# Optimization experiments

Hardware: AMD Instinct MI355X
Metric: run time of the kernel (lower is better)

The kernel has to match this reference:

```python
import jax, jax.numpy as jnp
import numpy as np

H = 512          # hidden_dim
D = 128          # input_dim
L = 8            # output_dim == NUMLABELS
T = 64           # encoder time steps per frame-feature sequence
W = 240          # WINDOWWIDTH (encoder batch dim, one element per frame)
CTX = W // 4     # 60 attention positions
NSTEPS = W // 8


def _lstm(x, Wih, Whh, bih, bhh):
    """PyTorch-convention LSTM (gate order i,f,g,o). x: (T,B,Din) -> (outputs (T,B,H), final h (B,H))."""
    B = x.shape[1]
    Hh = Whh.shape[1]
    xp = jnp.einsum('tbd,gd->tbg', x, Wih) + bih + bhh  # fold both biases
    def step(carry, g):
        h, c = carry
        g = g + h @ Whh.T
        i, f, gg, o = jnp.split(g, 4, axis=-1)
        c = jax.nn.sigmoid(f) * c + jax.nn.sigmoid(i) * jnp.tanh(gg)
        h = jax.nn.sigmoid(o) * jnp.tanh(c)
        return (h, c), h
    z = jnp.zeros((B, Hh), x.dtype)
    (hT, _), hs = jax.lax.scan(step, (z, z), xp)
    return hs, hT


def _forward(data, enc_Wih, enc_Whh, enc_bih, enc_bhh,
             p1f_Wih, p1f_Whh, p1f_bih, p1f_bhh, p1b_Wih, p1b_Whh, p1b_bih, p1b_bhh,
             p2f_Wih, p2f_Whh, p2f_bih, p2f_bhh, p2b_Wih, p2b_Whh, p2b_bih, p2b_bhh,
             attn_W, attn_b, comb_W, comb_b,
             gru_Wih, gru_Whh, gru_bih, gru_bhh, out_W, out_b):
    # --- encoder: per-frame LSTM over T steps, keep final hidden per frame ---
    _, h_enc = _lstm(data, enc_Wih, enc_Whh, enc_bih, enc_bhh)          # (W, H)
    # --- pyramidal bi-LSTM 1: pairs of frames ---
    x1 = h_enc.reshape(W // 2, 1, 2 * H)
    f1, _ = _lstm(x1, p1f_Wih, p1f_Whh, p1f_bih, p1f_bhh)
    b1, _ = _lstm(x1[::-1], p1b_Wih, p1b_Whh, p1b_bih, p1b_bhh)
    # --- pyramidal bi-LSTM 2 ---
    x2 = jnp.concatenate([f1, b1[::-1]], axis=-1).reshape(W // 4, 1, 4 * H)
    f2, h2T = _lstm(x2, p2f_Wih, p2f_Whh, p2f_bih, p2f_bhh)
    b2, _ = _lstm(x2[::-1], p2b_Wih, p2b_Whh, p2b_bih, p2b_bhh)
    ctx = jnp.concatenate([f2, b2[::-1]], axis=-1).reshape(CTX, 2 * H)  # (60, 2H)
    h = h2T[0]                                   # forward-direction final hidden, (H,)
    inp0 = jnp.zeros((L,), data.dtype).at[L - 1].set(1.0)  # one_hot(NOLABEL)

    def dec_step(carry, _):
        inp, h = carry
        aw = jax.nn.softmax(attn_W @ jnp.concatenate([inp, h]) + attn_b)    # (60,)
        applied = aw @ ctx                                                   # (2H,)
        o = jax.nn.relu(comb_W @ jnp.concatenate([inp, applied]) + comb_b)  # (H,)
        # PyTorch GRU cell (gate order r,z,n)
        gi = gru_Wih @ o + gru_bih
        gh = gru_Whh @ h + gru_bhh
        ir, iz, inn = jnp.split(gi, 3)
        hr, hz, hn = jnp.split(gh, 3)
        r = jax.nn.sigmoid(ir + hr)
        z = jax.nn.sigmoid(iz + hz)
        n = jnp.tanh(inn + r * hn)
        h_new = (1.0 - z) * n + z * h
        logp = jax.nn.log_softmax(out_W @ h_new + out_b)                     # (L,)
        return (logp, h_new), logp  # prediction feeds back as next input (y=None path)

    _, outputs = jax.lax.scan(dec_step, (inp0, h), None, length=NSTEPS)
    return outputs  # (30, L)


def setup_inputs() -> dict:
    key = jax.random.key(0)
    ks = iter(jax.random.split(key, 64))
    def mk(*shape):
        return (jax.random.normal(next(ks), shape) * 0.05).astype(jnp.float32)
    d = {"data": jax.random.normal(next(ks), (T, W, D), dtype=jnp.float32)}
    d.update(enc_Wih=mk(4 * H, D), enc_Whh=mk(4 * H, H), enc_bih=mk(4 * H), enc_bhh=mk(4 * H))
    for p, din in (("p1f", 2 * H), ("p1b", 2 * H), ("p2f", 4 * H), ("p2b", 4 * H)):
        d[p + "_Wih"] = mk(4 * H, din)
        d[p + "_Whh"] = mk(4 * H, H)
        d[p + "_bih"] = mk(4 * H)
        d[p + "_bhh"] = mk(4 * H)
    d.update(attn_W=mk(CTX, H + L), attn_b=mk(CTX), comb_W=mk(H, 2 * H + L), comb_b=mk(H),
             gru_Wih=mk(3 * H, H), gru_Whh=mk(3 * H, H), gru_bih=mk(3 * H), gru_bhh=mk(3 * H),
             out_W=mk(L, H), out_b=mk(L))
    return d


def reference(data, enc_Wih, enc_Whh, enc_bih, enc_bhh,
              p1f_Wih, p1f_Whh, p1f_bih, p1f_bhh, p1b_Wih, p1b_Whh, p1b_bih, p1b_bhh,
              p2f_Wih, p2f_Whh, p2f_bih, p2f_bhh, p2b_Wih, p2b_Whh, p2b_bih, p2b_bhh,
              attn_W, attn_b, comb_W, comb_b,
              gru_Wih, gru_Whh, gru_bih, gru_bhh, out_W, out_b):
    return _forward(data, enc_Wih, enc_Whh, enc_bih, enc_bhh,
                    p1f_Wih, p1f_Whh, p1f_bih, p1f_bhh, p1b_Wih, p1b_Whh, p1b_bih, p1b_bhh,
                    p2f_Wih, p2f_Whh, p2f_bih, p2f_bhh, p2b_Wih, p2b_Whh, p2b_bih, p2b_bhh,
                    attn_W, attn_b, comb_W, comb_b,
                    gru_Wih, gru_Whh, gru_bih, gru_bhh, out_W, out_b)
```

## Files before the change

kernel.cpp:

```cpp
#include <hip/hip_runtime.h>
#include <math.h>


typedef __attribute__((ext_vector_type(8))) short short8;
typedef __attribute__((ext_vector_type(4))) float floatx4;
typedef unsigned long long ull;

__device__ __forceinline__ float sigf(float x) { return 1.f / (1.f + __expf(-x)); }
__device__ __forceinline__ float tanh_f(float x) {
    float e = __expf(2.f * x);
    return 1.f - 2.f / (e + 1.f);
}
__device__ __forceinline__ unsigned short f2b(float x) {
    unsigned u = __float_as_uint(x);
    unsigned r = (u + 0x7FFFu + ((u >> 16) & 1u)) >> 16;
    return (unsigned short)r;
}

__device__ __forceinline__ float gld(const float* p) {
    return __hip_atomic_load(p, __ATOMIC_RELAXED, __HIP_MEMORY_SCOPE_AGENT);
}
__device__ __forceinline__ void gst(float* p, float v) {
    __hip_atomic_store(p, v, __ATOMIC_RELAXED, __HIP_MEMORY_SCOPE_AGENT);
}
__device__ __forceinline__ ull gldll(const ull* p) {
    return __hip_atomic_load(p, __ATOMIC_RELAXED, __HIP_MEMORY_SCOPE_AGENT);
}
__device__ __forceinline__ void gstll(ull* p, ull v) {
    __hip_atomic_store(p, v, __ATOMIC_RELAXED, __HIP_MEMORY_SCOPE_AGENT);
}
__device__ __forceinline__ ull packfe(float d, int ep) {
    return ((ull)(unsigned)ep << 32) | (ull)__float_as_uint(d);
}
__device__ __forceinline__ float lowf(ull v) { return __uint_as_float((unsigned)v); }

__global__ void init_k(float* __restrict__ ws) {
    for (int i = blockIdx.x * blockDim.x + threadIdx.x; i < 501760; i += gridDim.x * blockDim.x)
        ws[i] = 0.f;
}

__global__ void __launch_bounds__(256, 1) enc_all(
    const float* __restrict__ data,
    const float* __restrict__ Wih, const float* __restrict__ Whh,
    const float* __restrict__ bih, const float* __restrict__ bhh,
    ull* __restrict__ fastF,
    ull* __restrict__ hbufF,
    float* __restrict__ henc)
{
    __shared__ short act2[20 * 64 * 8];
    __shared__ float gw[4][640];
    __shared__ float cs[512];
    __shared__ short hw[4][16][8];
    __shared__ float biasL[4][4][8];

    const int tid = threadIdx.x;
    const int xcd = blockIdx.x & 7, kk = blockIdx.x >> 3;
    const int fg = xcd * 2 + (kk >> 4), ds = kk & 15;
    if (fg >= 15) return;

    const int w = tid >> 6, lane = tid & 63;
    const int n = lane & 15, q = lane >> 4;

    short8 bfrag[2][20];
#pragma unroll
    for (int nt = 0; nt < 2; ++nt) {
        int rr = nt * 16 + n;
        int g = rr >> 3, dp = rr & 7;
        int grow = g * 512 + ds * 32 + w * 8 + dp;
#pragma unroll
        for (int kt = 0; kt < 20; ++kt) {
            int k0 = kt * 32 + q * 8;
            const float* src = (k0 < 512) ? (Whh + (size_t)grow * 512 + k0)
                                          : (Wih + (size_t)grow * 128 + (k0 - 512));
            float4 lo = *(const float4*)src;
            float4 hi = *(const float4*)(src + 4);
            short8 bf;
            bf[0] = (short)f2b(lo.x); bf[1] = (short)f2b(lo.y);
            bf[2] = (short)f2b(lo.z); bf[3] = (short)f2b(lo.w);
            bf[4] = (short)f2b(hi.x); bf[5] = (short)f2b(hi.y);
            bf[6] = (short)f2b(hi.z); bf[7] = (short)f2b(hi.w);
            bfrag[nt][kt] = bf;
        }
    }
    if (tid < 128) {
        int w2 = tid >> 5, rr = tid & 31;
        int g = rr >> 3, dp = rr & 7;
        int grow = g * 512 + ds * 32 + w2 * 8 + dp;
        biasL[w2][g][dp] = bih[grow] + bhh[grow];
    }
    for (int i = tid; i < 512; i += 256) cs[i] = 0.f;
    __syncthreads();

    unsigned* a2u = (unsigned*)act2;

    for (int t = 0; t < 64; ++t) {
        const int kt2 = tid >> 6, l2 = tid & 63, f2v = l2 & 15, q2 = l2 >> 4;
        const float* xs = data + ((size_t)t * 240 + fg * 16 + f2v) * 128 + kt2 * 32 + q2 * 8;
        float4 lo = *(const float4*)xs;
        float4 hi = *(const float4*)(xs + 4);

        {
            const size_t goff = (size_t)((t & 1) * 15 + fg) * 4096;
            const ull* fsrc = fastF + goff;
            const ull* ssrc = hbufF + goff;
            ull v[16];
            for (;;) {
                bool ok = true;
#pragma unroll
                for (int k2 = 0; k2 < 16; ++k2) {
                    v[k2] = *(volatile const ull*)(fsrc + tid + 256 * k2);
                    ok &= ((int)(v[k2] >> 32) == t);
                }
                if (ok) break;
                ok = true;
#pragma unroll
                for (int k2 = 0; k2 < 16; ++k2) {
                    v[k2] = gldll(ssrc + tid + 256 * k2);
                    ok &= ((int)(v[k2] >> 32) == t);
                }
                if (ok) break;
                __builtin_amdgcn_s_sleep(1);
            }
#pragma unroll
            for (int k2 = 0; k2 < 16; ++k2)
                a2u[tid + 256 * k2] = (unsigned)v[k2];
        }
        {
            short8 xp;
            xp[0] = (short)f2b(lo.x); xp[1] = (short)f2b(lo.y);
            xp[2] = (short)f2b(lo.z); xp[3] = (short)f2b(lo.w);
            xp[4] = (short)f2b(hi.x); xp[5] = (short)f2b(hi.y);
            xp[6] = (short)f2b(hi.z); xp[7] = (short)f2b(hi.w);
            *(short8*)&act2[((16 + kt2) * 64 + l2) * 8] = xp;
        }
        __syncthreads();

        floatx4 acc0 = {0.f, 0.f, 0.f, 0.f};
        floatx4 acc1 = {0.f, 0.f, 0.f, 0.f};
#pragma unroll
        for (int kt = 0; kt < 20; ++kt) {
            short8 a = *(short8*)&act2[(kt * 64 + lane) * 8];
            acc0 = __builtin_amdgcn_mfma_f32_16x16x32_bf16(a, bfrag[0][kt], acc0, 0, 0, 0);
            acc1 = __builtin_amdgcn_mfma_f32_16x16x32_bf16(a, bfrag[1][kt], acc1, 0, 0, 0);
        }
        *(floatx4*)&gw[w][(0 * 16 + n) * 20 + 4 * q] = acc0;
        *(floatx4*)&gw[w][(1 * 16 + n) * 20 + 4 * q] = acc1;

        int nb = (t + 1) & 1;
#pragma unroll
        for (int it = 0; it < 2; ++it) {
            int f = lane & 15, dp = q + 4 * it;
            float gi = gw[w][(0 * 8 + dp) * 20 + f] + biasL[w][0][dp];
            float gf = gw[w][(1 * 8 + dp) * 20 + f] + biasL[w][1][dp];
            float gg = gw[w][(2 * 8 + dp) * 20 + f] + biasL[w][2][dp];
            float go = gw[w][(3 * 8 + dp) * 20 + f] + biasL[w][3][dp];
            int ci = f * 32 + w * 8 + dp;
            float cc = cs[ci];
            float cn = sigf(gf) * cc + sigf(gi) * tanh_f(gg);
            float hn = sigf(go) * tanh_f(cn);
            cs[ci] = cn;
            hw[w][f][dp] = (short)f2b(hn);
            if (t == 63)
                gst(&henc[(size_t)(fg * 16 + f) * 512 + ds * 32 + w * 8 + dp], hn);
        }
        if (lane < 16) {
            const unsigned* hwu = (const unsigned*)&hw[w][lane][0];
            size_t off = (size_t)(nb * 15 + fg) * 4096 + (ds * 64 + w * 16 + lane) * 4;
            ull* fdst = fastF + off;
            ull* sdst = hbufF + off;
            const ull ep = ((ull)(unsigned)(t + 1)) << 32;
#pragma unroll
            for (int r = 0; r < 4; ++r) {
                ull wv = ep | (ull)hwu[r];
                *(volatile ull*)(fdst + r) = wv;
                gstll(sdst + r, wv);
            }
        }
        __syncthreads();
    }
}

__global__ void __launch_bounds__(256) gemm_xp2(
    const float* __restrict__ A, int M, int K, int halfgrid,
    const float* __restrict__ WvF, const float* __restrict__ baF,
    const float* __restrict__ bbF, float* __restrict__ CF,
    const float* __restrict__ WvB, const float* __restrict__ baB,
    const float* __restrict__ bbB, float* __restrict__ CB)
{
    __shared__ float At[16][66];
    __shared__ float Wt[128][66];
    const int tid = threadIdx.x;
    int bgl = blockIdx.x;
    const int rev = (bgl >= halfgrid) ? 1 : 0;
    if (rev) bgl -= halfgrid;
    const float* Wv = rev ? WvB : WvF;
    const float* ba = rev ? baB : baF;
    const float* bb = rev ? bbB : bbF;
    float* C        = rev ? CB : CF;

    const int nt = bgl & 15, mt = bgl >> 4;
    const int rp = tid >> 2, fq = tid & 3;
    const int lr0 = 2 * rp, lr1 = lr0 + 1;
    const int n0 = nt * 128 + lr0, n1 = n0 + 1;

    float acc0[4], acc1[4];
    {
        float b0 = ba[n0] + bb[n0], b1 = ba[n1] + bb[n1];
#pragma unroll
        for (int j = 0; j < 4; ++j) { acc0[j] = b0; acc1[j] = b1; }
    }

    for (int kt = 0; kt < K; kt += 64) {
        {
            int f = tid >> 4, c4 = tid & 15;
            int m = mt * 16 + f;
            float4 v = make_float4(0.f, 0.f, 0.f, 0.f);
            if (m < M) {
                int ar = rev ? (M - 1 - m) : m;
                v = ((const float4*)(A + (size_t)ar * K + kt))[c4];
            }
            At[f][c4 * 4 + 0] = v.x; At[f][c4 * 4 + 1] = v.y;
            At[f][c4 * 4 + 2] = v.z; At[f][c4 * 4 + 3] = v.w;
        }
        for (int i = tid; i < 2048; i += 256) {
            int lr = i >> 4, c4 = i & 15;
            float4 v = ((const float4*)(Wv + (size_t)(nt * 128 + lr) * K + kt))[c4];
            Wt[lr][c4 * 4 + 0] = v.x; Wt[lr][c4 * 4 + 1] = v.y;
            Wt[lr][c4 * 4 + 2] = v.z; Wt[lr][c4 * 4 + 3] = v.w;
        }
        __syncthreads();
        const float2* w0p = (const float2*)(&Wt[lr0][0]);
        const float2* w1p = (const float2*)(&Wt[lr1][0]);
#pragma unroll 8
        for (int kh = 0; kh < 32; ++kh) {
            float2 w0 = w0p[kh], w1 = w1p[kh];
#pragma unroll
            for (int j = 0; j < 4; ++j) {
                float2 av = ((const float2*)(&At[4 * fq + j][0]))[kh];
                acc0[j] += w0.x * av.x + w0.y * av.y;
                acc1[j] += w1.x * av.x + w1.y * av.y;
            }
        }
        __syncthreads();
    }
#pragma unroll
    for (int j = 0; j < 4; ++j) {
        int m = mt * 16 + 4 * fq + j;
        if (m < M) {
            C[(size_t)m * 2048 + n0] = acc0[j];
            C[(size_t)m * 2048 + n1] = acc1[j];
        }
    }
}

__global__ void __launch_bounds__(256, 1) pyr_rec(
    const float* __restrict__ xpF, const float* __restrict__ xpB,
    const float* __restrict__ WhhF, const float* __restrict__ WhhB,
    ull* __restrict__ hp,
    float* __restrict__ outF, float* __restrict__ outB,
    int steps)
{
    const int tid = threadIdx.x;
    const int dir = blockIdx.x >> 6, blk = blockIdx.x & 63;
    const float* xp  = dir ? xpB : xpF;
    const float* Whh = dir ? WhhB : WhhF;
    float* outp = dir ? outB : outF;
    ull* hpd = hp + (size_t)dir * 1024;

    __shared__ __align__(16) float hcur[512];
    __shared__ float red[32][9];
    __shared__ float gv[32];

    const int lr = tid & 31, seg = tid >> 5;
    const int grow = (lr >> 3) * 512 + blk * 8 + (lr & 7);
    float4 wl4[16];
#pragma unroll
    for (int j = 0; j < 16; ++j)
        wl4[j] = *(const float4*)&Whh[(size_t)grow * 512 + 4 * seg + 32 * j];

    const int growx = (tid >> 3) * 512 + blk * 8 + (tid & 7);
    float creg = 0.f;
    __syncthreads();

    for (int t = 0; t < steps; ++t) {
        float xg = 0.f;
        if (tid < 32) xg = xp[(size_t)t * 2048 + growx];
        {
            const ull* base = hpd + (size_t)(t & 1) * 512;
            ull v0 = gldll(base + tid), v1 = gldll(base + tid + 256);
            while (((int)(v0 >> 32) != t) | ((int)(v1 >> 32) != t)) {
                __builtin_amdgcn_s_sleep(1);
                v0 = gldll(base + tid);
                v1 = gldll(base + tid + 256);
            }
            hcur[tid]       = lowf(v0);
            hcur[tid + 256] = lowf(v1);
        }
        __syncthreads();

        float a = 0.f;
#pragma unroll
        for (int j = 0; j < 16; ++j) {
            float4 w = wl4[j];
            float4 h4 = *(const float4*)&hcur[4 * seg + 32 * j];
            a += w.x*h4.x + w.y*h4.y + w.z*h4.z + w.w*h4.w;
        }
        red[lr][seg] = a;
        __syncthreads();

        if (tid < 32) {
            float g = xg;
#pragma unroll
            for (int s2 = 0; s2 < 8; ++s2) g += red[tid][s2];
            gv[tid] = g;
        }
        __syncthreads();
        if (tid < 8) {
            float i_ = sigf(gv[tid]), f_ = sigf(gv[8 + tid]);
            float g_ = tanh_f(gv[16 + tid]), o_ = sigf(gv[24 + tid]);
            creg = f_ * creg + i_ * g_;
            float hn = o_ * tanh_f(creg);
            int d = blk * 8 + tid;
            gstll(&hpd[((t + 1) & 1) * 512 + d], packfe(hn, t + 1));
            int row = dir ? (steps - 1 - t) : t;
            outp[(size_t)row * 512 + d] = hn;
        }
        __syncthreads();
    }
}

__global__ void x2_assemble(const float* __restrict__ f1, const float* __restrict__ b1o,
                            float* __restrict__ x2)
{
    int j = blockIdx.x;
    for (int k = threadIdx.x; k < 2048; k += 256) {
        int q = k >> 9, r = k & 511;
        const float* src = (q & 1) ? b1o : f1;
        int row = 2 * j + (q >> 1);
        x2[(size_t)j * 2048 + k] = src[(size_t)row * 512 + r];
    }
}

__global__ void ctx_k(const float* __restrict__ f2, const float* __restrict__ b2o,
                      float* __restrict__ ctx, ull* __restrict__ hdec_p)
{
    int j = blockIdx.x;
    for (int k = threadIdx.x; k < 1024; k += 256)
        ctx[(size_t)j * 1024 + k] = (k < 512) ? f2[(size_t)j * 512 + k]
                                              : b2o[(size_t)j * 512 + k - 512];
    if (j == 0) {
        for (int i = threadIdx.x; i < 512; i += 256)
            hdec_p[i] = packfe(f2[59 * 512 + i], 0);
    }
}

__global__ void __launch_bounds__(256) precomp_M(
    const float* __restrict__ comb_W,
    const float* __restrict__ ctx,
    float* __restrict__ MgT)
{
    __shared__ float cw[8 * 1024];
    const int tid = threadIdx.x, d0 = blockIdx.x * 8;
    for (int i = tid; i < 2048; i += 256) {
        int r = i >> 8, c4 = i & 255;
        float4 v = *(const float4*)&comb_W[(size_t)(d0 + r) * 1032 + 8 + 4 * c4];
        *(float4*)&cw[r * 1024 + 4 * c4] = v;
    }
    __syncthreads();
    for (int o = tid; o < 480; o += 256) {
        int dl = o / 60, j = o % 60;
        const float4* cp = (const float4*)&cw[dl * 1024];
        const float4* xp = (const float4*)(ctx + (size_t)j * 1024);
        float a = 0.f;
#pragma unroll 4
        for (int k = 0; k < 256; ++k) {
            float4 w = cp[k], x = xp[k];
            a += w.x * x.x + w.y * x.y + w.z * x.z + w.w * x.w;
        }
        MgT[(size_t)j * 512 + (d0 + dl)] = a;
    }
}

__global__ void __launch_bounds__(512, 1) dec_k(
    const float* __restrict__ attn_W, const float* __restrict__ attn_b,
    const float* __restrict__ comb_W, const float* __restrict__ comb_b,
    const float* __restrict__ gWih, const float* __restrict__ gWhh,
    const float* __restrict__ gbih, const float* __restrict__ gbhh,
    const float* __restrict__ outW, const float* __restrict__ outb,
    const float* __restrict__ MgT,
    ull* __restrict__ hdec_p,
    float* __restrict__ dout)
{
    const int tid = threadIdx.x, bid = blockIdx.x;
    const int lane = tid & 63, wv = tid >> 6;
    const int dbase = bid * 8;

    __shared__ float M2T[68][512];
    __shared__ __align__(16) float hL[520];
    __shared__ __align__(16) float xl[512];
    __shared__ __align__(16) float awx[68];
    __shared__ float zd[8], zh[64];
    __shared__ float ghl[24], gil[24];
    __shared__ float biasg[24], biasi[24];
    __shared__ float cbL[512];
    __shared__ float attnbL[64], outbL[8];

    const int rg = tid >> 4, sg = tid & 15;
    const int rz = tid >> 3, szz = tid & 7;

    float4 wo2[2];
    float4 wg8[8], wi8[8];
    float4 wzh[16];
    float4 wip[2];
    {
        const float* wp = outW + (size_t)wv * 512 + 4 * lane;
        wo2[0] = *(const float4*)wp;
        wo2[1] = *(const float4*)(wp + 256);
    }
    {
        int rr = (rg < 24) ? rg : 23;
        size_t grow = (size_t)((rr >> 3) * 512 + dbase + (rr & 7)) * 512 + 4 * sg;
#pragma unroll
        for (int i = 0; i < 8; ++i) {
            wg8[i] = *(const float4*)&gWhh[grow + 64 * i];
            wi8[i] = *(const float4*)&gWih[grow + 64 * i];
        }
    }
    {
        int rr = (rz < 60) ? rz : 59;
        size_t base = (size_t)rr * 520 + 8 + 4 * szz;
#pragma unroll
        for (int i = 0; i < 16; ++i)
            wzh[i] = *(const float4*)&attn_W[base + 32 * i];
    }
    {
        int rr = (tid < 60) ? tid : 59;
        wip[0] = *(const float4*)&attn_W[(size_t)rr * 520 + 0];
        wip[1] = *(const float4*)&attn_W[(size_t)rr * 520 + 4];
    }
    if (tid < 24) {
        int g2 = (tid >> 3) * 512 + dbase + (tid & 7);
        biasg[tid] = gbhh[g2];
        biasi[tid] = gbih[g2];
    }
    cbL[tid] = comb_b[tid];
    if (tid < 64) attnbL[tid] = (tid < 60) ? attn_b[tid] : 0.f;
    if (tid < 8) outbL[tid] = outb[tid];
    for (int i = tid; i < 7680; i += 512) {
        int j = i >> 7, c4 = i & 127;
        *(float4*)&M2T[j][4 * c4] = *(const float4*)&MgT[(size_t)j * 512 + 4 * c4];
    }
    for (int i = tid; i < 4096; i += 512) {
        int r = i >> 3, c = i & 7;
        M2T[60 + c][r] = comb_W[(size_t)r * 1032 + c];
    }
    __syncthreads();

    for (int s = 0; s < 30; ++s) {
        {
            const ull* hs = hdec_p + (size_t)(s & 1) * 512;
            ull v0 = gldll(hs + tid);
            while ((int)(v0 >> 32) != s) {
                __builtin_amdgcn_s_sleep(1);
                v0 = gldll(hs + tid);
            }
            hL[tid] = lowf(v0);
        }
        __syncthreads();

        {
            float a = 0.f;
            float4 h0 = *(const float4*)&hL[4 * lane];
            float4 h1 = *(const float4*)&hL[4 * lane + 256];
            a += wo2[0].x*h0.x + wo2[0].y*h0.y + wo2[0].z*h0.z + wo2[0].w*h0.w;
            a += wo2[1].x*h1.x + wo2[1].y*h1.y + wo2[1].z*h1.z + wo2[1].w*h1.w;
#pragma unroll
            for (int off = 32; off; off >>= 1) a += __shfl_xor(a, off);
            if (lane == 0) zd[wv] = a;
        }
        {
            float a = 0.f;
#pragma unroll
            for (int i = 0; i < 8; ++i) {
                float4 w = wg8[i];
                float4 h4 = *(const float4*)&hL[4 * sg + 64 * i];
                a += w.x*h4.x + w.y*h4.y + w.z*h4.z + w.w*h4.w;
            }
            a += __shfl_xor(a, 1); a += __shfl_xor(a, 2);
            a += __shfl_xor(a, 4); a += __shfl_xor(a, 8);
            if (sg == 0 && rg < 24) ghl[rg] = a;
        }
        {
            float a = 0.f;
#pragma unroll
            for (int i = 0; i < 16; ++i) {
                float4 w = wzh[i];
                float4 h4 = *(const float4*)&hL[4 * szz + 32 * i];
                a += w.x*h4.x + w.y*h4.y + w.z*h4.z + w.w*h4.w;
            }
            a += __shfl_xor(a, 1); a += __shfl_xor(a, 2); a += __shfl_xor(a, 4);
            if (szz == 0 && rz < 60) zh[rz] = a;
        }
        __syncthreads();

        if (wv == 0) {
            if (lane < 8) {
                float v;
                if (s > 0) {
                    float a = zd[lane] + outbL[lane];
                    float m = a;
                    m = fmaxf(m, __shfl_xor(m, 1));
                    m = fmaxf(m, __shfl_xor(m, 2));
                    m = fmaxf(m, __shfl_xor(m, 4));
                    float e = __expf(a - m);
                    float ss2 = e;
                    ss2 += __shfl_xor(ss2, 1);
                    ss2 += __shfl_xor(ss2, 2);
                    ss2 += __shfl_xor(ss2, 4);
                    v = a - m - __logf(ss2);
                    if (bid == 0) dout[(s - 1) * 8 + lane] = v;
                } else {
                    v = (lane == 7) ? 1.f : 0.f;
                }
                awx[60 + lane] = v;
            }
            float z = -1e30f;
            if (lane < 60) {
                z = zh[lane] + attnbL[lane]
                  + wip[0].x * awx[60] + wip[0].y * awx[61]
                  + wip[0].z * awx[62] + wip[0].w * awx[63]
                  + wip[1].x * awx[64] + wip[1].y * awx[65]
                  + wip[1].z * awx[66] + wip[1].w * awx[67];
            }
            float m = z;
#pragma unroll
            for (int off = 32; off; off >>= 1) m = fmaxf(m, __shfl_xor(m, off));
            float e = (lane < 60) ? __expf(z - m) : 0.f;
            float ss2 = e;
#pragma unroll
            for (int off = 32; off; off >>= 1) ss2 += __shfl_xor(ss2, off);
            if (lane < 60) awx[lane] = e / ss2;
        }
        __syncthreads();

        {
            float a = cbL[tid];
#pragma unroll 4
            for (int k = 0; k < 68; ++k)
                a += M2T[k][tid] * awx[k];
            xl[tid] = fmaxf(a, 0.f);
        }
        __syncthreads();

        {
            float a = 0.f;
#pragma unroll
            for (int i = 0; i < 8; ++i) {
                float4 w = wi8[i];
                float4 o4 = *(const float4*)&xl[4 * sg + 64 * i];
                a += w.x*o4.x + w.y*o4.y + w.z*o4.z + w.w*o4.w;
            }
            a += __shfl_xor(a, 1); a += __shfl_xor(a, 2);
            a += __shfl_xor(a, 4); a += __shfl_xor(a, 8);
            if (sg == 0 && rg < 24) gil[rg] = a;
        }
        __syncthreads();

        if (tid < 8) {
            float gh0 = biasg[tid] + ghl[tid];
            float gh1 = biasg[8 + tid] + ghl[8 + tid];
            float gh2 = biasg[16 + tid] + ghl[16 + tid];
            float gi0 = biasi[tid] + gil[tid];
            float gi1 = biasi[8 + tid] + gil[8 + tid];
            float gi2 = biasi[16 + tid] + gil[16 + tid];
            float r_ = sigf(gi0 + gh0);
            float z_ = sigf(gi1 + gh1);
            float n_ = tanh_f(gi2 + r_ * gh2);
            float hnew = (1.f - z_) * n_ + z_ * hL[dbase + tid];
            gstll(&hdec_p[(size_t)((s + 1) & 1) * 512 + dbase + tid], packfe(hnew, s + 1));
        }
        __syncthreads();
    }

    if (bid == 0) {
        {
            const ull* hs = hdec_p + (size_t)(30 & 1) * 512;
            ull v0 = gldll(hs + tid);
            while ((int)(v0 >> 32) != 30) {
                __builtin_amdgcn_s_sleep(1);
                v0 = gldll(hs + tid);
            }
            hL[tid] = lowf(v0);
        }
        __syncthreads();
        {
            float a = 0.f;
            float4 h0 = *(const float4*)&hL[4 * lane];
            float4 h1 = *(const float4*)&hL[4 * lane + 256];
            a += wo2[0].x*h0.x + wo2[0].y*h0.y + wo2[0].z*h0.z + wo2[0].w*h0.w;
            a += wo2[1].x*h1.x + wo2[1].y*h1.y + wo2[1].z*h1.z + wo2[1].w*h1.w;
#pragma unroll
            for (int off = 32; off; off >>= 1) a += __shfl_xor(a, off);
            if (lane == 0) zd[wv] = a;
        }
        __syncthreads();
        if (tid < 8) {
            float a = zd[tid] + outbL[tid];
            float m = a;
            m = fmaxf(m, __shfl_xor(m, 1));
            m = fmaxf(m, __shfl_xor(m, 2));
            m = fmaxf(m, __shfl_xor(m, 4));
            float e = __expf(a - m);
            float ss2 = e;
            ss2 += __shfl_xor(ss2, 1);
            ss2 += __shfl_xor(ss2, 2);
            ss2 += __shfl_xor(ss2, 4);
            dout[29 * 8 + tid] = a - m - __logf(ss2);
        }
    }
}

extern "C" void kernel_launch(void* const* d_in, const int* in_sizes, int n_in,
                              void* d_out, int out_size, void* d_ws, size_t ws_size,
                              hipStream_t stream) {
    (void)in_sizes; (void)n_in; (void)out_size; (void)ws_size;
    const float* data    = (const float*)d_in[0];
    const float* enc_Wih = (const float*)d_in[1];
    const float* enc_Whh = (const float*)d_in[2];
    const float* enc_bih = (const float*)d_in[3];
    const float* enc_bhh = (const float*)d_in[4];
    const float* p1f_Wih = (const float*)d_in[5];
    const float* p1f_Whh = (const float*)d_in[6];
    const float* p1f_bih = (const float*)d_in[7];
    const float* p1f_bhh = (const float*)d_in[8];
    const float* p1b_Wih = (const float*)d_in[9];
    const float* p1b_Whh = (const float*)d_in[10];
    const float* p1b_bih = (const float*)d_in[11];
    const float* p1b_bhh = (const float*)d_in[12];
    const float* p2f_Wih = (const float*)d_in[13];
    const float* p2f_Whh = (const float*)d_in[14];
    const float* p2f_bih = (const float*)d_in[15];
    const float* p2f_bhh = (const float*)d_in[16];
    const float* p2b_Wih = (const float*)d_in[17];
    const float* p2b_Whh = (const float*)d_in[18];
    const float* p2b_bih = (const float*)d_in[19];
    const float* p2b_bhh = (const float*)d_in[20];
    const float* attn_W  = (const float*)d_in[21];
    const float* attn_b  = (const float*)d_in[22];
    const float* comb_W  = (const float*)d_in[23];
    const float* comb_b  = (const float*)d_in[24];
    const float* gru_Wih = (const float*)d_in[25];
    const float* gru_Whh = (const float*)d_in[26];
    const float* gru_bih = (const float*)d_in[27];
    const float* gru_bhh = (const float*)d_in[28];
    const float* out_W   = (const float*)d_in[29];
    const float* out_b   = (const float*)d_in[30];

    float* ws = (float*)d_ws;
    ull* fastF   = (ull*)ws;
    ull* hbufF   = (ull*)(ws + 245760);
    ull* hp1     = (ull*)(ws + 491520);
    ull* hp2     = (ull*)(ws + 495616);
    ull* hdec_p  = (ull*)(ws + 499712);
    float* henc  = ws + 501760;
    float* xp1f  = ws + 624640;
    float* xp1b  = ws + 870400;
    float* f1    = ws + 1116160;
    float* b1o   = ws + 1177600;
    float* x2    = ws + 1239040;
    float* xp2f  = ws + 1361920;
    float* xp2b  = ws + 1484800;
    float* f2    = ws + 1607680;
    float* b2o   = ws + 1638400;
    float* ctxb  = ws + 1669120;
    float* MgT   = ws + 1730560;

    init_k<<<256, 256, 0, stream>>>(ws);

    enc_all<<<256, 256, 0, stream>>>(data, enc_Wih, enc_Whh, enc_bih, enc_bhh,
                                     fastF, hbufF, henc);
    gemm_xp2<<<256, 256, 0, stream>>>(henc, 120, 1024, 128,
                                      p1f_Wih, p1f_bih, p1f_bhh, xp1f,
                                      p1b_Wih, p1b_bih, p1b_bhh, xp1b);
    pyr_rec<<<128, 256, 0, stream>>>(xp1f, xp1b, p1f_Whh, p1b_Whh, hp1, f1, b1o, 120);
    x2_assemble<<<60, 256, 0, stream>>>(f1, b1o, x2);
    gemm_xp2<<<128, 256, 0, stream>>>(x2, 60, 2048, 64,
                                      p2f_Wih, p2f_bih, p2f_bhh, xp2f,
                                      p2b_Wih, p2b_bih, p2b_bhh, xp2b);
    pyr_rec<<<128, 256, 0, stream>>>(xp2f, xp2b, p2f_Whh, p2b_Whh, hp2, f2, b2o, 60);
    ctx_k<<<60, 256, 0, stream>>>(f2, b2o, ctxb, hdec_p);
    precomp_M<<<64, 256, 0, stream>>>(comb_W, ctxb, MgT);
    dec_k<<<64, 512, 0, stream>>>(attn_W, attn_b, comb_W, comb_b,
                                  gru_Wih, gru_Whh, gru_bih, gru_bhh,
                                  out_W, out_b, MgT, hdec_p,
                                  (float*)d_out);
}
```

Measured before the change: 1.442 ms.

## Assign encoder work by hardware XCD id via atomic claim counters

Instead of assuming the block-to-XCD mapping from blockIdx, each encoder block reads its real XCC id from a hardware register, claims a slot with an atomic counter, waits for all 256 blocks to register, and computes a dense work index so that frame groups sharing h-state stay on the same XCD. This keeps the fast-path exchange buffer local to one L2. It also adds a credit counter that stops polling the fast buffer after repeated misses and falls back to the coherent buffer. The cost is a grid-wide startup barrier, which relies on all blocks being co-resident.

```diff
diff --git a/kernel.cpp b/kernel.cpp
--- a/kernel.cpp
+++ b/kernel.cpp
@@ -29,13 +29,18 @@
 __device__ __forceinline__ void gstll(ull* p, ull v) {
     __hip_atomic_store(p, v, __ATOMIC_RELAXED, __HIP_MEMORY_SCOPE_AGENT);
 }
+__device__ __forceinline__ int gldi(const int* p) {
+    return __hip_atomic_load(p, __ATOMIC_RELAXED, __HIP_MEMORY_SCOPE_AGENT);
+}
 __device__ __forceinline__ ull packfe(float d, int ep) {
     return ((ull)(unsigned)ep << 32) | (ull)__float_as_uint(d);
 }
 __device__ __forceinline__ float lowf(ull v) { return __uint_as_float((unsigned)v); }
 
+#define XCC_GETREG_IMM ((3 << 11) | (0 << 6) | 20)
+
 __global__ void init_k(float* __restrict__ ws) {
-    for (int i = blockIdx.x * blockDim.x + threadIdx.x; i < 501760; i += gridDim.x * blockDim.x)
+    for (int i = blockIdx.x * blockDim.x + threadIdx.x; i < 501776; i += gridDim.x * blockDim.x)
         ws[i] = 0.f;
 }
 
@@ -45,18 +50,36 @@
     const float* __restrict__ bih, const float* __restrict__ bhh,
     ull* __restrict__ fastF,
     ull* __restrict__ hbufF,
-    float* __restrict__ henc)
+    float* __restrict__ henc,
+    int* __restrict__ claim)
 {
     __shared__ short act2[20 * 64 * 8];
     __shared__ float gw[4][640];
     __shared__ float cs[512];
     __shared__ short hw[4][16][8];
     __shared__ float biasL[4][4][8];
+    __shared__ int sWork;
 
     const int tid = threadIdx.x;
-    const int xcd = blockIdx.x & 7, kk = blockIdx.x >> 3;
-    const int fg = xcd * 2 + (kk >> 4), ds = kk & 15;
-    if (fg >= 15) return;
+
+    if (tid == 0) {
+        unsigned xcd = __builtin_amdgcn_s_getreg(XCC_GETREG_IMM) & 7u;
+        int slot = __hip_atomic_fetch_add(&claim[xcd], 1, __ATOMIC_RELAXED,
+                                          __HIP_MEMORY_SCOPE_AGENT);
+        __hip_atomic_fetch_add(&claim[8], 1 + (slot >> 20), __ATOMIC_RELAXED,
+                               __HIP_MEMORY_SCOPE_AGENT);
+        while (gldi(&claim[8]) < 256) __builtin_amdgcn_s_sleep(1);
+        int pre = 0;
+        for (int x = 0; x < 8; ++x) {
+            int c = gldi(&claim[x]);
+            if (x < (int)xcd) pre += c;
+        }
+        sWork = pre + slot;
+    }
+    __syncthreads();
+    const int work = sWork;
+    if (work >= 240) return;
+    const int fg = work >> 4, ds = work & 15;
 
     const int w = tid >> 6, lane = tid & 63;
     const int n = lane & 15, q = lane >> 4;
@@ -92,6 +115,7 @@
     __syncthreads();
 
     unsigned* a2u = (unsigned*)act2;
+    int fastOK = 1, fcredit = 3;
 
     for (int t = 0; t < 64; ++t) {
         const int kt2 = tid >> 6, l2 = tid & 63, f2v = l2 & 15, q2 = l2 >> 4;
@@ -104,22 +128,30 @@
             const ull* fsrc = fastF + goff;
             const ull* ssrc = hbufF + goff;
             ull v[16];
+            bool gotFast = false;
             for (;;) {
-                bool ok = true;
-#pragma unroll
-                for (int k2 = 0; k2 < 16; ++k2) {
-                    v[k2] = *(volatile const ull*)(fsrc + tid + 256 * k2);
-                    ok &= ((int)(v[k2] >> 32) == t);
+                if (fastOK) {
+                    bool ok = true;
+#pragma unroll
+                    for (int k2 = 0; k2 < 16; ++k2) {
+                        v[k2] = *(volatile const ull*)(fsrc + tid + 256 * k2);
+                        ok &= ((int)(v[k2] >> 32) == t);
+                    }
+                    if (ok) { gotFast = true; break; }
                 }
-                if (ok) break;
-                ok = true;
-#pragma unroll
-                for (int k2 = 0; k2 < 16; ++k2) {
-                    v[k2] = gldll(ssrc + tid + 256 * k2);
-                    ok &= ((int)(v[k2] >> 32) == t);
+                {
+                    bool ok = true;
+#pragma unroll
+                    for (int k2 = 0; k2 < 16; ++k2) {
+                        v[k2] = gldll(ssrc + tid + 256 * k2);
+                        ok &= ((int)(v[k2] >> 32) == t);
+                    }
+                    if (ok) break;
                 }
-                if (ok) break;
                 __builtin_amdgcn_s_sleep(1);
+            }
+            if (fastOK && !gotFast) {
+                if (--fcredit <= 0) fastOK = 0;
             }
 #pragma unroll
             for (int k2 = 0; k2 < 16; ++k2)
@@ -662,23 +694,24 @@
     ull* hp1     = (ull*)(ws + 491520);
     ull* hp2     = (ull*)(ws + 495616);
     ull* hdec_p  = (ull*)(ws + 499712);
-    float* henc  = ws + 501760;
-    float* xp1f  = ws + 624640;
-    float* xp1b  = ws + 870400;
-    float* f1    = ws + 1116160;
-    float* b1o   = ws + 1177600;
-    float* x2    = ws + 1239040;
-    float* xp2f  = ws + 1361920;
-    float* xp2b  = ws + 1484800;
-    float* f2    = ws + 1607680;
-    float* b2o   = ws + 1638400;
-    float* ctxb  = ws + 1669120;
-    float* MgT   = ws + 1730560;
+    int* claimC  = (int*)(ws + 501760);
+    float* henc  = ws + 501776;
+    float* xp1f  = ws + 624656;
+    float* xp1b  = ws + 870416;
+    float* f1    = ws + 1116176;
+    float* b1o   = ws + 1177616;
+    float* x2    = ws + 1239056;
+    float* xp2f  = ws + 1361936;
+    float* xp2b  = ws + 1484816;
+    float* f2    = ws + 1607696;
+    float* b2o   = ws + 1638416;
+    float* ctxb  = ws + 1669136;
+    float* MgT   = ws + 1730576;
 
     init_k<<<256, 256, 0, stream>>>(ws);
 
     enc_all<<<256, 256, 0, stream>>>(data, enc_Wih, enc_Whh, enc_bih, enc_bhh,
-                                     fastF, hbufF, henc);
+                                     fastF, hbufF, henc, claimC);
     gemm_xp2<<<256, 256, 0, stream>>>(henc, 120, 1024, 128,
                                       p1f_Wih, p1f_bih, p1f_bhh, xp1f,
                                       p1b_Wih, p1b_bih, p1b_bhh, xp1b);
```

After: 1.439 ms. No clear change (-0.3%).
